# Kernel optimization log

Measured on AMD Instinct MI355X. Metric: run time of the kernel, lower is better.

## Reference

```python
import jax, jax.numpy as jnp
import numpy as np

N_COLS = 107
CAT_SLICES = [(1, 10), (10, 26), (27, 34), (34, 49), (49, 55), (55, 60), (60, 62), (65, 107)]
MSE_COLS = [0, 26, 62, 63, 64]
BATCH = 524288


def setup_inputs() -> dict:
    key = jax.random.key(0)
    k_dec, k_cont, k_cat = jax.random.split(key, 3)
    data_decoded = jax.random.normal(k_dec, (BATCH, N_COLS), dtype=jnp.float32)
    # Build data_true: continuous cols random, categorical slices exactly one-hot.
    data_true = jax.random.uniform(k_cont, (BATCH, N_COLS), dtype=jnp.float32)
    rows = jnp.arange(BATCH)
    for i, (s, e) in enumerate(CAT_SLICES):
        kk = jax.random.fold_in(k_cat, i)
        labels = jax.random.randint(kk, (BATCH,), 0, e - s)
        data_true = data_true.at[:, s:e].set(0.0)
        data_true = data_true.at[rows, s + labels].set(1.0)
    return {"data_decoded": data_decoded, "data_true": data_true, "batch_size": BATCH}


def _ce(logits, onehot_true):
    # torch nonzero()[:,1] on an exact one-hot slice == argmax
    labels = jnp.argmax(onehot_true, axis=1)
    logp = jax.nn.log_softmax(logits, axis=1)
    return -jnp.mean(jnp.take_along_axis(logp, labels[:, None], axis=1))


def _mse(a, b):
    d = a - b
    return jnp.mean(d * d)


def reference(data_decoded, data_true, batch_size):
    mse_loss = jnp.float32(0.0)
    for c in MSE_COLS:
        mse_loss = mse_loss + _mse(data_decoded[:, c], data_true[:, c])
    ce_loss = jnp.float32(0.0)
    for s, e in CAT_SLICES:
        ce_loss = ce_loss + _ce(data_decoded[:, s:e], data_true[:, s:e])
    multi_loss = mse_loss + ce_loss
    return multi_loss, mse_loss, ce_loss
```

## Files before the change

kernel.cpp:

```cpp
#include <hip/hip_runtime.h>

#define NCOLS 107
#define ROWS_PER_GROUP 4
#define GROUP_F4 NCOLS
#define THREADS 256

typedef float f4 __attribute__((ext_vector_type(4)));

__device__ __host__ __forceinline__ constexpr int slice_of(int col) {
    return (col >= 1  && col < 10) ? 0 :
           (col >= 10 && col < 26) ? 1 :
           (col >= 27 && col < 34) ? 2 :
           (col >= 34 && col < 49) ? 3 :
           (col >= 49 && col < 55) ? 4 :
           (col >= 55 && col < 60) ? 5 :
           (col >= 60 && col < 62) ? 6 :
           (col >= 65)             ? 7 : -1;
}
__device__ __host__ __forceinline__ constexpr int slice_last(int sid) {
    return sid == 0 ?  9 : sid == 1 ? 25 : sid == 2 ? 33 : sid == 3 ? 48 :
           sid == 4 ? 54 : sid == 5 ? 59 : sid == 6 ? 61 : 106;
}

template<int L>
__device__ __forceinline__ void elem(float d, float t, float (&s)[8],
                                     float& mse, float& dot, float& lse) {
    constexpr int col = L % NCOLS;
    constexpr int sid = slice_of(col);
    if constexpr (sid < 0) {
        float df = d - t;
        mse += df * df;
    } else {
        s[sid] += __expf(d);
        dot = __builtin_fmaf(d, t, dot);
        if constexpr (col == slice_last(sid)) {
            lse += __logf(s[sid]);
            s[sid] = 0.0f;
        }
    }
}

template<int C>
__device__ __forceinline__ void walk(const f4* __restrict__ gd,
                                     const f4* __restrict__ gt,
                                     float (&s)[8],
                                     float& mse, float& dot, float& lse) {
    if constexpr (C < GROUP_F4) {
        f4 dv = gd[C];
        f4 tv = gt[C];
        elem<4 * C + 0>(dv[0], tv[0], s, mse, dot, lse);
        elem<4 * C + 1>(dv[1], tv[1], s, mse, dot, lse);
        elem<4 * C + 2>(dv[2], tv[2], s, mse, dot, lse);
        elem<4 * C + 3>(dv[3], tv[3], s, mse, dot, lse);
        walk<C + 1>(gd, gt, s, mse, dot, lse);
    }
}

__global__ __launch_bounds__(THREADS, 2) void multiloss_main(
        const float* __restrict__ dec, const float* __restrict__ tru,
        float2* __restrict__ ws, int ngroups) {
    int g = blockIdx.x * THREADS + threadIdx.x;
    float mse = 0.0f, dot = 0.0f, lse = 0.0f;
    float s[8] = {0.0f, 0.0f, 0.0f, 0.0f, 0.0f, 0.0f, 0.0f, 0.0f};
    if (g < ngroups) {
        const f4* gd = (const f4*)dec + (size_t)g * GROUP_F4;
        const f4* gt = (const f4*)tru + (size_t)g * GROUP_F4;
        walk<0>(gd, gt, s, mse, dot, lse);
    }
    float ce = lse - dot;
#pragma unroll
    for (int off = 32; off > 0; off >>= 1) {
        mse += __shfl_down(mse, off, 64);
        ce  += __shfl_down(ce,  off, 64);
    }
    int lane  = threadIdx.x & 63;
    int gwave = (blockIdx.x * THREADS + threadIdx.x) >> 6;
    if (lane == 0)
        ws[gwave] = make_float2(mse, ce);
}

__global__ __launch_bounds__(256) void multiloss_fin(
        const float2* __restrict__ ws, float* __restrict__ out,
        int nslots, float invN) {
    float m = 0.0f, c = 0.0f;
    for (int i = threadIdx.x; i < nslots; i += 256) {
        float2 v = ws[i];
        m += v.x; c += v.y;
    }
#pragma unroll
    for (int off = 32; off > 0; off >>= 1) {
        m += __shfl_down(m, off, 64);
        c += __shfl_down(c, off, 64);
    }
    __shared__ float sm[4], sc[4];
    int wid  = threadIdx.x >> 6;
    int lane = threadIdx.x & 63;
    if (lane == 0) { sm[wid] = m; sc[wid] = c; }
    __syncthreads();
    if (threadIdx.x == 0) {
        float mse = (sm[0] + sm[1] + sm[2] + sm[3]) * invN;
        float ce  = (sc[0] + sc[1] + sc[2] + sc[3]) * invN;
        out[0] = mse + ce;
        out[1] = mse;
        out[2] = ce;
    }
}

extern "C" void kernel_launch(void* const* d_in, const int* in_sizes, int n_in,
                              void* d_out, int out_size, void* d_ws, size_t ws_size,
                              hipStream_t stream) {
    const float* dec = (const float*)d_in[0];
    const float* tru = (const float*)d_in[1];
    int nrows   = in_sizes[0] / NCOLS;
    int ngroups = nrows / ROWS_PER_GROUP;
    int nblocks = (ngroups + THREADS - 1) / THREADS;
    int nwaves  = nblocks * (THREADS / 64);
    float2* ws = (float2*)d_ws;
    multiloss_main<<<nblocks, THREADS, 0, stream>>>(dec, tru, ws, ngroups);
    multiloss_fin<<<1, 256, 0, stream>>>(ws, (float*)d_out, nwaves,
                                         1.0f / (float)nrows);
}
```

Baseline: 520.1 us.

## Software-pipeline per-thread loads in batches with three-deep prefetch

```diff
diff --git a/kernel.cpp b/kernel.cpp
--- a/kernel.cpp
+++ b/kernel.cpp
@@ -4,8 +4,15 @@
 #define ROWS_PER_GROUP 4
 #define GROUP_F4 NCOLS
 #define THREADS 256
+#define BN 4
+#define NBAT 27
 
 typedef float f4 __attribute__((ext_vector_type(4)));
+
+__device__ __host__ __forceinline__ constexpr int bstart(int b) { return b * BN; }
+__device__ __host__ __forceinline__ constexpr int blen(int b) {
+    return b < NBAT - 1 ? BN : (GROUP_F4 - BN * (NBAT - 1));
+}
 
 __device__ __host__ __forceinline__ constexpr int slice_of(int col) {
     return (col >= 1  && col < 10) ? 0 :
@@ -40,19 +47,48 @@
     }
 }
 
-template<int C>
-__device__ __forceinline__ void walk(const f4* __restrict__ gd,
-                                     const f4* __restrict__ gt,
-                                     float (&s)[8],
-                                     float& mse, float& dot, float& lse) {
-    if constexpr (C < GROUP_F4) {
-        f4 dv = gd[C];
-        f4 tv = gt[C];
-        elem<4 * C + 0>(dv[0], tv[0], s, mse, dot, lse);
-        elem<4 * C + 1>(dv[1], tv[1], s, mse, dot, lse);
-        elem<4 * C + 2>(dv[2], tv[2], s, mse, dot, lse);
-        elem<4 * C + 3>(dv[3], tv[3], s, mse, dot, lse);
-        walk<C + 1>(gd, gt, s, mse, dot, lse);
+
+template<int B, int K = 0>
+__device__ __forceinline__ void bload(const f4* __restrict__ gd,
+                                      const f4* __restrict__ gt,
+                                      f4 (&d)[BN], f4 (&t)[BN]) {
+    if constexpr (K < blen(B)) {
+        d[K] = gd[bstart(B) + K];
+        t[K] = gt[bstart(B) + K];
+        bload<B, K + 1>(gd, gt, d, t);
+    }
+}
+
+template<int B, int K = 0>
+__device__ __forceinline__ void bproc(const f4 (&d)[BN], const f4 (&t)[BN],
+                                      float (&s)[8],
+                                      float& mse, float& dot, float& lse) {
+    if constexpr (K < blen(B)) {
+        constexpr int C = bstart(B) + K;
+        elem<4 * C + 0>(d[K][0], t[K][0], s, mse, dot, lse);
+        elem<4 * C + 1>(d[K][1], t[K][1], s, mse, dot, lse);
+        elem<4 * C + 2>(d[K][2], t[K][2], s, mse, dot, lse);
+        elem<4 * C + 3>(d[K][3], t[K][3], s, mse, dot, lse);
+        bproc<B, K + 1>(d, t, s, mse, dot, lse);
+    }
+}
+
+template<int B>
+__device__ __forceinline__ void stage(const f4* __restrict__ gd,
+                                      const f4* __restrict__ gt,
+                                      f4 (&d0)[BN], f4 (&t0)[BN],
+                                      f4 (&d1)[BN], f4 (&t1)[BN],
+                                      f4 (&d2)[BN], f4 (&t2)[BN],
+                                      float (&s)[8],
+                                      float& mse, float& dot, float& lse) {
+    f4 d3[BN], t3[BN];
+    if constexpr (B + 3 < NBAT) {
+        bload<B + 3>(gd, gt, d3, t3);
+        __builtin_amdgcn_sched_barrier(0);
+    }
+    bproc<B>(d0, t0, s, mse, dot, lse);
+    if constexpr (B + 1 < NBAT) {
+        stage<B + 1>(gd, gt, d1, t1, d2, t2, d3, t3, s, mse, dot, lse);
     }
 }
 
@@ -65,7 +101,11 @@
     if (g < ngroups) {
         const f4* gd = (const f4*)dec + (size_t)g * GROUP_F4;
         const f4* gt = (const f4*)tru + (size_t)g * GROUP_F4;
-        walk<0>(gd, gt, s, mse, dot, lse);
+        f4 ad[BN], at[BN], bd[BN], bt[BN], cd[BN], ct[BN];
+        bload<0>(gd, gt, ad, at);
+        bload<1>(gd, gt, bd, bt);
+        bload<2>(gd, gt, cd, ct);
+        stage<0>(gd, gt, ad, at, bd, bt, cd, ct, s, mse, dot, lse);
     }
     float ce = lse - dot;
 #pragma unroll
```

After: 463.8 us. 1.12x faster.
